# Kernel optimization log

Measured on AMD Instinct MI355X. Metric: run time of the kernel, lower is better.

Reference implementation:

```python
import jax, jax.numpy as jnp
import numpy as np

L, N, K, F, H = 6, 32768, 8, 32, 256  # levels, nodes/level, fan-in, feat_dim, hidden_dim


def setup_inputs() -> dict:
    key = jax.random.key(0)
    ks = jax.random.split(key, 10)
    sc = lambda k, shape, fan: (jax.random.normal(k, shape, jnp.float32) / np.sqrt(fan).astype(np.float32))
    return {
        "feats": jax.random.normal(ks[0], (L, N, F), jnp.float32),
        "pred_idx": jax.random.randint(ks[1], (L - 1, N, K), 0, N),
        "We": sc(ks[2], (H, F), F),
        "be": jnp.zeros((H,), jnp.float32),
        "rs_W1": sc(ks[3], (12, H, H), H),
        "rs_b1": jnp.zeros((12, H), jnp.float32),
        "rs_W2": sc(ks[4], (12, H, H), H),
        "rs_b2": jnp.zeros((12, H), jnp.float32),
        "rs_W3": sc(ks[5], (12, H, H), H),
        "rs_b3": jnp.zeros((12, H), jnp.float32),
        "rc_W1": sc(ks[6], (6, 2 * H, 2 * H), 2 * H),
        "rc_b1": jnp.zeros((6, 2 * H), jnp.float32),
        "rc_W2": sc(ks[7], (6, 2 * H, 2 * H), 2 * H),
        "rc_b2": jnp.zeros((6, 2 * H), jnp.float32),
        "rc_W3": sc(ks[8], (6, H, 2 * H), 2 * H),
        "rc_b3": jnp.zeros((6, H), jnp.float32),
    }


def _resnet(W1, b1, W2, b2, W3, b3, x):
    # lay3(tanh(lay2(tanh(lay1(x)))) + x)
    h1 = jnp.tanh(x @ W1.T + b1)
    h2 = jnp.tanh(h1 @ W2.T + b2)
    return (h2 + x) @ W3.T + b3


def reference(feats, pred_idx, We, be,
              rs_W1, rs_b1, rs_W2, rs_b2, rs_W3, rs_b3,
              rc_W1, rc_b1, rc_W2, rc_b2, rc_W3, rc_b3):
    # rs (h,h,h) order: [d1_mp, d1_mp1, d2_mp, d2_mp1, d3_mp, d3_mp1,
    #                    d1_node1, d2_node1, d3_node1, d1_comb1, d2_comb1, d3_comb1]
    # rc (2h,2h,h) order: [d1_node, d2_node, d3_node, d1_comb, d2_comb, d3_comb]
    small = lambda i, x: _resnet(rs_W1[i], rs_b1[i], rs_W2[i], rs_b2[i], rs_W3[i], rs_b3[i], x)
    big = lambda i, x: _resnet(rc_W1[i], rc_b1[i], rc_W2[i], rc_b2[i], rc_W3[i], rc_b3[i], x)

    n_levels = feats.shape[0]
    embeds = []
    for l in range(n_levels):  # sequential topological dependency (fixed, small L)
        e = jnp.tanh(feats[l] @ We.T + be)  # embed_op
        if l > 0:
            d = min(l - 1, 2)  # bwd_depth -> d1/d2/d3 branch
            # comb_embed branch: 'bwd_node_embeds' field exists but is DGL's
            # zero-initialized default for this frontier -> concat with zeros.
            x = jnp.concatenate([e, jnp.zeros_like(e)], axis=-1)
            e = jnp.tanh(small(9 + d, jnp.tanh(big(3 + d, x))))
            # message: gather predecessor embeds, sum-reduce, mp resnets
            msgs = jnp.sum(embeds[l - 1][pred_idx[l - 1]], axis=1)  # [N, H]
            r = jnp.tanh(small(2 * d, msgs))
            r = jnp.tanh(small(2 * d + 1, r))
            # node_embeds branch: concat(embeds, msgs_redux)
            x2 = jnp.concatenate([e, r], axis=-1)
            e = jnp.tanh(small(6 + d, jnp.tanh(big(d, x2))))
        embeds.append(e)
    return jnp.stack(embeds)  # graph.ndata['bwd_node_embeds'], [L, N, H]
```

## Files before the change

kernel.cpp:

```cpp
#include <hip/hip_runtime.h>

#define NLVL 6
#define NN   32768
#define KFAN 8
#define FDIM 32
#define HDIM 256

typedef __attribute__((ext_vector_type(4))) float f32x4;
typedef __attribute__((ext_vector_type(8))) _Float16 f16x8;
typedef __attribute__((ext_vector_type(4))) unsigned short u16x4;

__device__ __forceinline__ float h2f(unsigned short u) {
    _Float16 h; __builtin_memcpy(&h, &u, 2); return (float)h;
}
__device__ __forceinline__ unsigned short f2h(float f) {
    _Float16 h = (_Float16)f;
    unsigned short u; __builtin_memcpy(&u, &h, 2); return u;
}
__device__ __forceinline__ float tanh_fast(float x) {
    float e = __expf(2.0f * x);
    return 1.0f - 2.0f / (e + 1.0f);
}
__device__ __forceinline__ void gload16(const void* g, void* l) {
    __builtin_amdgcn_global_load_lds((const __attribute__((address_space(1))) void*)g,
                                     (__attribute__((address_space(3))) void*)l, 16, 0, 0);
}

template<bool RES, bool F32OUT>
__global__ __launch_bounds__(256)
void gemm_bt(const unsigned short* __restrict__ A, int lda,
             const unsigned short* __restrict__ B, int ldb,
             const float* __restrict__ bias,
             const unsigned short* __restrict__ res, int ldr,
             unsigned short* __restrict__ outB, int ldo,
             float* __restrict__ outF,
             int K)
{
    __shared__ __align__(16) unsigned short sA[128 * 64];
    __shared__ __align__(16) unsigned short sB[128 * 64];

    const int tid  = threadIdx.x;
    const int wid  = tid >> 6;
    const int lane = tid & 63;
    const int wr   = wid >> 1, wc = wid & 1;
    const int brow = blockIdx.x * 128;
    const int bcol = blockIdx.y * 128;
    const int fr   = lane & 15, fq = lane >> 4;
    const int srow = lane >> 3;
    const int scol = ((lane & 7) ^ srow) * 8;

    f32x4 acc[4][4] = {};

    for (int k0 = 0; k0 < K; k0 += 64) {
        #pragma unroll
        for (int it = 0; it < 4; ++it) {
            const int c = wid * 4 + it;
            const int r = c * 8 + srow;
            gload16(A + (size_t)(brow + r) * lda + k0 + scol, sA + c * 512);
            gload16(B + (size_t)(bcol + r) * ldb + k0 + scol, sB + c * 512);
        }
        __syncthreads();
        #pragma unroll
        for (int ks = 0; ks < 2; ++ks) {
            f16x8 av[4], bv[4];
            #pragma unroll
            for (int m = 0; m < 4; ++m) {
                const int r = wr * 64 + m * 16 + fr;
                const int b = r * 128 + ((ks * 64 + fq * 16) ^ ((r & 7) << 4));
                av[m] = *(const f16x8*)((const char*)sA + b);
            }
            #pragma unroll
            for (int n = 0; n < 4; ++n) {
                const int r = wc * 64 + n * 16 + fr;
                const int b = r * 128 + ((ks * 64 + fq * 16) ^ ((r & 7) << 4));
                bv[n] = *(const f16x8*)((const char*)sB + b);
            }
            #pragma unroll
            for (int m = 0; m < 4; ++m)
                #pragma unroll
                for (int n = 0; n < 4; ++n)
                    acc[m][n] = __builtin_amdgcn_mfma_f32_16x16x32_f16(av[m], bv[n], acc[m][n], 0, 0, 0);
        }
        __syncthreads();
    }

    #pragma unroll
    for (int m = 0; m < 4; ++m) {
        #pragma unroll
        for (int n = 0; n < 4; ++n) {
            const int col = bcol + wc * 64 + n * 16 + fr;
            const float bb = bias[col];
            #pragma unroll
            for (int j = 0; j < 4; ++j) {
                const int row = brow + wr * 64 + m * 16 + fq * 4 + j;
                float v = acc[m][n][j] + bb;
                v = tanh_fast(v);
                if (RES) v += h2f(res[(size_t)row * ldr + col]);
                outB[(size_t)row * ldo + col] = f2h(v);
                if (F32OUT) outF[(size_t)row * HDIM + col] = v;
            }
        }
    }
}

template<bool ZERO2, bool F32OUT>
__global__ __launch_bounds__(256)
void embed_kernel(const float* __restrict__ feats,
                  const float* __restrict__ We,
                  const float* __restrict__ be,
                  unsigned short* __restrict__ outB, int ldo,
                  float* __restrict__ outF)
{
    __shared__ float sW[256 * 33];
    __shared__ float sF[16 * 32];
    const int t = threadIdx.x;
    #pragma unroll
    for (int i = 0; i < 32; ++i) {
        int idx = t + 256 * i;
        sW[(idx >> 5) * 33 + (idx & 31)] = We[idx];
    }
    const size_t base = (size_t)blockIdx.x * 16;
    for (int i = t; i < 16 * 32; i += 256) sF[i] = feats[base * 32 + i];
    __syncthreads();

    const float bb = be[t];
    for (int r = 0; r < 16; ++r) {
        float a = bb;
        #pragma unroll
        for (int k = 0; k < 32; ++k) a += sF[r * 32 + k] * sW[t * 33 + k];
        const float v = tanh_fast(a);
        const size_t row = base + r;
        outB[row * ldo + t] = f2h(v);
        if (ZERO2) outB[row * ldo + 256 + t] = 0;
        if (F32OUT) outF[row * HDIM + t] = v;
    }
}

__global__ __launch_bounds__(256)
void gather_kernel(const unsigned short* __restrict__ ehalf,
                   const int* __restrict__ idx,
                   unsigned short* __restrict__ msg)
{
    const int n = blockIdx.x;
    const int t = threadIdx.x;
    const int* row = idx + (size_t)n * KFAN;
    float s = 0.f;
    #pragma unroll
    for (int k = 0; k < KFAN; ++k)
        s += h2f(ehalf[(size_t)row[k] * HDIM + t]);
    msg[(size_t)n * HDIM + t] = f2h(s);
}

__global__ __launch_bounds__(256)
void cvt_kernel(const float* __restrict__ in, unsigned short* __restrict__ out, int n4)
{
    const int i = blockIdx.x * 256 + threadIdx.x;
    if (i >= n4) return;
    const float4 v = ((const float4*)in)[i];
    u16x4 o;
    o[0] = f2h(v.x); o[1] = f2h(v.y); o[2] = f2h(v.z); o[3] = f2h(v.w);
    ((u16x4*)out)[i] = o;
}

extern "C" void kernel_launch(void* const* d_in, const int* in_sizes, int n_in,
                              void* d_out, int out_size, void* d_ws, size_t ws_size,
                              hipStream_t stream)
{
    const float* feats    = (const float*)d_in[0];
    const int*   pred_idx = (const int*)d_in[1];
    const float* We       = (const float*)d_in[2];
    const float* be       = (const float*)d_in[3];
    const float* rs_W1    = (const float*)d_in[4];
    const float* rs_b1    = (const float*)d_in[5];
    const float* rs_W2    = (const float*)d_in[6];
    const float* rs_b2    = (const float*)d_in[7];
    const float* rs_W3    = (const float*)d_in[8];
    const float* rs_b3    = (const float*)d_in[9];
    const float* rc_W1    = (const float*)d_in[10];
    const float* rc_b1    = (const float*)d_in[11];
    const float* rc_W2    = (const float*)d_in[12];
    const float* rc_b2    = (const float*)d_in[13];
    const float* rc_W3    = (const float*)d_in[14];
    const float* rc_b3    = (const float*)d_in[15];
    float* out = (float*)d_out;

    char* ws = (char*)d_ws;
    size_t off = 0;
    auto alloc = [&](size_t bytes) -> unsigned short* {
        unsigned short* p = (unsigned short*)(ws + off);
        off += (bytes + 255) & ~(size_t)255;
        return p;
    };
    unsigned short* rcW1b = alloc((size_t)6 * 512 * 512 * 2);
    unsigned short* rcW2b = alloc((size_t)6 * 512 * 512 * 2);
    unsigned short* rcW3b = alloc((size_t)6 * 256 * 512 * 2);
    unsigned short* rsW1b = alloc((size_t)12 * 256 * 256 * 2);
    unsigned short* rsW2b = alloc((size_t)12 * 256 * 256 * 2);
    unsigned short* rsW3b = alloc((size_t)12 * 256 * 256 * 2);
    unsigned short* xcat  = alloc((size_t)NN * 512 * 2);
    unsigned short* p0    = alloc((size_t)NN * 512 * 2);
    unsigned short* p1    = alloc((size_t)NN * 512 * 2);
    unsigned short* Tb    = alloc((size_t)NN * 256 * 2);
    unsigned short* q0    = alloc((size_t)NN * 256 * 2);
    unsigned short* q1    = alloc((size_t)NN * 256 * 2);
    unsigned short* msgb  = alloc((size_t)NN * 256 * 2);
    unsigned short* ebfA  = alloc((size_t)NN * 256 * 2);
    unsigned short* ebfB  = alloc((size_t)NN * 256 * 2);
    (void)ws_size; (void)in_sizes; (void)n_in; (void)out_size;

    auto cvt = [&](const float* src, unsigned short* dst, int n) {
        int n4 = n / 4;
        cvt_kernel<<<dim3((n4 + 255) / 256), dim3(256), 0, stream>>>(src, dst, n4);
    };
    cvt(rc_W1, rcW1b, 6 * 512 * 512);
    cvt(rc_W2, rcW2b, 6 * 512 * 512);
    cvt(rc_W3, rcW3b, 6 * 256 * 512);
    cvt(rs_W1, rsW1b, 12 * 256 * 256);
    cvt(rs_W2, rsW2b, 12 * 256 * 256);
    cvt(rs_W3, rsW3b, 12 * 256 * 256);

    auto G = [&](const unsigned short* Ap, int Kd, const unsigned short* Bp, int Nout,
                 const float* bp, const unsigned short* rp, int ldr,
                 unsigned short* ob, int ldo, float* of) {
        dim3 grid(NN / 128, Nout / 128);
        if (of)
            gemm_bt<false, true><<<grid, dim3(256), 0, stream>>>(Ap, Kd, Bp, Kd, bp, nullptr, 0, ob, ldo, of, Kd);
        else if (rp)
            gemm_bt<true, false><<<grid, dim3(256), 0, stream>>>(Ap, Kd, Bp, Kd, bp, rp, ldr, ob, ldo, nullptr, Kd);
        else
            gemm_bt<false, false><<<grid, dim3(256), 0, stream>>>(Ap, Kd, Bp, Kd, bp, nullptr, 0, ob, ldo, nullptr, Kd);
    };

    unsigned short* ebp = ebfA;
    unsigned short* ebc = ebfB;

    embed_kernel<false, true><<<dim3(NN / 16), dim3(256), 0, stream>>>(
        feats, We, be, ebp, 256, out);

    for (int l = 1; l < NLVL; ++l) {
        const int d = (l - 1 < 2) ? (l - 1) : 2;
        const float* fl = feats + (size_t)l * NN * FDIM;

        embed_kernel<true, false><<<dim3(NN / 16), dim3(256), 0, stream>>>(
            fl, We, be, xcat, 512, nullptr);

        G(xcat, 512, rcW1b + (size_t)(3 + d) * 512 * 512, 512, rc_b1 + (3 + d) * 512, nullptr, 0, p0, 512, nullptr);
        G(p0,   512, rcW2b + (size_t)(3 + d) * 512 * 512, 512, rc_b2 + (3 + d) * 512, xcat, 512,  p1, 512, nullptr);
        G(p1,   512, rcW3b + (size_t)(3 + d) * 256 * 512, 256, rc_b3 + (3 + d) * 256, nullptr, 0, Tb, 256, nullptr);
        G(Tb,   256, rsW1b + (size_t)(9 + d) * 256 * 256, 256, rs_b1 + (9 + d) * 256, nullptr, 0, q0, 256, nullptr);
        G(q0,   256, rsW2b + (size_t)(9 + d) * 256 * 256, 256, rs_b2 + (9 + d) * 256, Tb, 256,   q1, 256, nullptr);
        G(q1,   256, rsW3b + (size_t)(9 + d) * 256 * 256, 256, rs_b3 + (9 + d) * 256, nullptr, 0, p0, 512, nullptr);

        gather_kernel<<<dim3(NN), dim3(256), 0, stream>>>(
            ebp, pred_idx + (size_t)(l - 1) * NN * KFAN, msgb);
        G(msgb, 256, rsW1b + (size_t)(2 * d) * 256 * 256,     256, rs_b1 + (2 * d) * 256,     nullptr, 0, q0, 256, nullptr);
        G(q0,   256, rsW2b + (size_t)(2 * d) * 256 * 256,     256, rs_b2 + (2 * d) * 256,     msgb, 256,  q1, 256, nullptr);
        G(q1,   256, rsW3b + (size_t)(2 * d) * 256 * 256,     256, rs_b3 + (2 * d) * 256,     nullptr, 0, Tb, 256, nullptr);
        G(Tb,   256, rsW1b + (size_t)(2 * d + 1) * 256 * 256, 256, rs_b1 + (2 * d + 1) * 256, nullptr, 0, q0, 256, nullptr);
        G(q0,   256, rsW2b + (size_t)(2 * d + 1) * 256 * 256, 256, rs_b2 + (2 * d + 1) * 256, Tb, 256,   q1, 256, nullptr);
        G(q1,   256, rsW3b + (size_t)(2 * d + 1) * 256 * 256, 256, rs_b3 + (2 * d + 1) * 256, nullptr, 0, p0 + 256, 512, nullptr);

        G(p0,   512, rcW1b + (size_t)d * 512 * 512, 512, rc_b1 + d * 512, nullptr, 0, p1,   512, nullptr);
        G(p1,   512, rcW2b + (size_t)d * 512 * 512, 512, rc_b2 + d * 512, p0, 512,   xcat, 512, nullptr);
        G(xcat, 512, rcW3b + (size_t)d * 256 * 512, 256, rc_b3 + d * 256, nullptr, 0, Tb,  256, nullptr);
        G(Tb,   256, rsW1b + (size_t)(6 + d) * 256 * 256, 256, rs_b1 + (6 + d) * 256, nullptr, 0, q0, 256, nullptr);
        G(q0,   256, rsW2b + (size_t)(6 + d) * 256 * 256, 256, rs_b2 + (6 + d) * 256, Tb, 256,   q1, 256, nullptr);
        G(q1,   256, rsW3b + (size_t)(6 + d) * 256 * 256, 256, rs_b3 + (6 + d) * 256, nullptr, 0, ebc, 256,
          out + (size_t)l * NN * HDIM);

        unsigned short* tmp = ebp; ebp = ebc; ebc = tmp;
    }
}
```

Baseline: 2.073 ms.

## Fuse each three-layer resnet into one LDS-resident kernel with gather and zero-half skip

Replaces the per-layer GEMM launches with a single kernel per resnet block. The input tile and the hidden activations stay in shared memory across all three layers, and the weight fragments are read directly from global memory with double-buffered register prefetch. The predecessor gather-sum now runs inside the first message-passing resnet, and the big comb resnet uses K=256 because the concatenated second half is structurally zero. This removes most intermediate HBM round-trips and kernel launches, at the cost of large LDS footprints that limit occupancy and uncached global weight loads in the inner loop.

```diff
diff --git a/kernel.cpp b/kernel.cpp
--- a/kernel.cpp
+++ b/kernel.cpp
@@ -26,84 +26,183 @@
                                      (__attribute__((address_space(3))) void*)l, 16, 0, 0);
 }
 
-template<bool RES, bool F32OUT>
-__global__ __launch_bounds__(256)
-void gemm_bt(const unsigned short* __restrict__ A, int lda,
-             const unsigned short* __restrict__ B, int ldb,
-             const float* __restrict__ bias,
-             const unsigned short* __restrict__ res, int ldr,
-             unsigned short* __restrict__ outB, int ldo,
-             float* __restrict__ outF,
-             int K)
-{
-    __shared__ __align__(16) unsigned short sA[128 * 64];
-    __shared__ __align__(16) unsigned short sB[128 * 64];
-
-    const int tid  = threadIdx.x;
-    const int wid  = tid >> 6;
-    const int lane = tid & 63;
-    const int wr   = wid >> 1, wc = wid & 1;
-    const int brow = blockIdx.x * 128;
-    const int bcol = blockIdx.y * 128;
-    const int fr   = lane & 15, fq = lane >> 4;
-    const int srow = lane >> 3;
-    const int scol = ((lane & 7) ^ srow) * 8;
-
-    f32x4 acc[4][4] = {};
-
-    for (int k0 = 0; k0 < K; k0 += 64) {
-        #pragma unroll
-        for (int it = 0; it < 4; ++it) {
-            const int c = wid * 4 + it;
-            const int r = c * 8 + srow;
-            gload16(A + (size_t)(brow + r) * lda + k0 + scol, sA + c * 512);
-            gload16(B + (size_t)(bcol + r) * ldb + k0 + scol, sB + c * 512);
+template<int KLEN, int ROWB, int MFR>
+__device__ __forceinline__ void layer_mm(const unsigned short* sA,
+                                         const unsigned short* __restrict__ Wg, int ldw,
+                                         int rbase, int wcol, int lane,
+                                         f32x4 (&acc)[MFR][4])
+{
+    const int fr = lane & 15, fq = lane >> 4;
+    #pragma unroll
+    for (int m = 0; m < MFR; ++m)
+        #pragma unroll
+        for (int n = 0; n < 4; ++n)
+            acc[m][n] = (f32x4){0.f, 0.f, 0.f, 0.f};
+
+    constexpr int NKS = KLEN / 32;
+    f16x8 avA[MFR], avB[MFR], bvA[4], bvB[4];
+
+    auto ldB = [&](int ks, f16x8* bv) {
+        #pragma unroll
+        for (int n = 0; n < 4; ++n)
+            bv[n] = *(const f16x8*)(Wg + (size_t)(wcol + n * 16 + fr) * ldw + ks * 32 + fq * 8);
+    };
+    auto ldA = [&](int ks, f16x8* av) {
+        #pragma unroll
+        for (int m = 0; m < MFR; ++m) {
+            const int rr = rbase + m * 16 + fr;
+            const int byt = rr * ROWB + ((ks * 64 + fq * 16) ^ ((rr & 7) << 4));
+            av[m] = *(const f16x8*)((const char*)sA + byt);
         }
+    };
+    auto mm = [&](f16x8* av, f16x8* bv) {
+        #pragma unroll
+        for (int m = 0; m < MFR; ++m)
+            #pragma unroll
+            for (int n = 0; n < 4; ++n)
+                acc[m][n] = __builtin_amdgcn_mfma_f32_16x16x32_f16(av[m], bv[n], acc[m][n], 0, 0, 0);
+    };
+
+    ldA(0, avA); ldB(0, bvA);
+    #pragma unroll
+    for (int s = 0; s < NKS / 2; ++s) {
+        ldA(2 * s + 1, avB); ldB(2 * s + 1, bvB);
+        mm(avA, bvA);
+        if (2 * s + 2 < NKS) { ldA(2 * s + 2, avA); ldB(2 * s + 2, bvA); }
+        mm(avB, bvB);
+    }
+}
+
+template<int BM, int KD, int K1, bool GATHER, bool F32OUT>
+__global__ __launch_bounds__(512, 2)
+void resnet_fused(const unsigned short* __restrict__ X, int ldx,
+                  const int* __restrict__ gidx,
+                  const unsigned short* __restrict__ gsrc,
+                  const unsigned short* __restrict__ W1, const float* __restrict__ b1,
+                  const unsigned short* __restrict__ W2, const float* __restrict__ b2,
+                  const unsigned short* __restrict__ W3, const float* __restrict__ b3,
+                  unsigned short* __restrict__ outB, int ldo,
+                  float* __restrict__ outF)
+{
+    __shared__ __align__(16) unsigned short sX[BM * K1];
+    __shared__ __align__(16) unsigned short sH[BM * KD];
+    constexpr int ROWBX = K1 * 2, ROWBH = KD * 2;
+
+    const int tid = threadIdx.x, lane = tid & 63, wid = tid >> 6;
+    const int brow = blockIdx.x * BM;
+    const int fr = lane & 15, fq = lane >> 4;
+
+    if (GATHER) {
+        constexpr int CB = K1 / 8;
+        for (int i = tid; i < BM * CB; i += 512) {
+            const int row = i / CB, cb = i % CB;
+            const int* ip = gidx + (size_t)(brow + row) * KFAN;
+            float s[8] = {0.f, 0.f, 0.f, 0.f, 0.f, 0.f, 0.f, 0.f};
+            #pragma unroll
+            for (int k = 0; k < KFAN; ++k) {
+                f16x8 v = *(const f16x8*)(gsrc + (size_t)ip[k] * HDIM + cb * 8);
+                #pragma unroll
+                for (int j = 0; j < 8; ++j) s[j] += (float)v[j];
+            }
+            f16x8 o;
+            #pragma unroll
+            for (int j = 0; j < 8; ++j) o[j] = (_Float16)s[j];
+            *(f16x8*)((char*)sX + row * ROWBX + ((cb * 16) ^ ((row & 7) << 4))) = o;
+        }
+    } else {
+        constexpr int ROUNDS = BM * K1 * 2 / (512 * 16);
+        #pragma unroll
+        for (int r = 0; r < ROUNDS; ++r) {
+            const int lin = (r * 512 + tid) * 16;
+            const int row = lin / ROWBX;
+            const int cb  = (lin % ROWBX) >> 4;
+            const int scb = cb ^ (row & 7);
+            gload16(X + (size_t)(brow + row) * ldx + scb * 8,
+                    (char*)sX + (lin - lane * 16));
+        }
+    }
+    __syncthreads();
+
+    constexpr int NWC12 = KD / 64;
+    const int wc12 = (wid % NWC12) * 64;
+    const int rb12 = (wid / NWC12) * 64;
+    {
+        f32x4 a1[4][4];
+        layer_mm<K1, ROWBX, 4>(sX, W1, KD, rb12, wc12, lane, a1);
+        #pragma unroll
+        for (int m = 0; m < 4; ++m)
+            #pragma unroll
+            for (int n = 0; n < 4; ++n) {
+                const int col = wc12 + n * 16 + fr;
+                const float bb = b1[col];
+                #pragma unroll
+                for (int j = 0; j < 4; ++j) {
+                    const int row = rb12 + m * 16 + fq * 4 + j;
+                    const float v = tanh_fast(a1[m][n][j] + bb);
+                    *(unsigned short*)((char*)sH + row * ROWBH + ((col * 2) ^ ((row & 7) << 4))) = f2h(v);
+                }
+            }
+    }
+    __syncthreads();
+
+    {
+        f32x4 a2[4][4];
+        layer_mm<KD, ROWBH, 4>(sH, W2, KD, rb12, wc12, lane, a2);
+        #pragma unroll
+        for (int m = 0; m < 4; ++m)
+            #pragma unroll
+            for (int n = 0; n < 4; ++n) {
+                const int col = wc12 + n * 16 + fr;
+                const float bb = b2[col];
+                #pragma unroll
+                for (int j = 0; j < 4; ++j) {
+                    const int row = rb12 + m * 16 + fq * 4 + j;
+                    float v = tanh_fast(a2[m][n][j] + bb);
+                    if (col < K1)
+                        v += h2f(*(const unsigned short*)((const char*)sX + row * ROWBX + ((col * 2) ^ ((row & 7) << 4))));
+                    a2[m][n][j] = v;
+                }
+            }
         __syncthreads();
         #pragma unroll
-        for (int ks = 0; ks < 2; ++ks) {
-            f16x8 av[4], bv[4];
-            #pragma unroll
-            for (int m = 0; m < 4; ++m) {
-                const int r = wr * 64 + m * 16 + fr;
-                const int b = r * 128 + ((ks * 64 + fq * 16) ^ ((r & 7) << 4));
-                av[m] = *(const f16x8*)((const char*)sA + b);
-            }
+        for (int m = 0; m < 4; ++m)
             #pragma unroll
             for (int n = 0; n < 4; ++n) {
-                const int r = wc * 64 + n * 16 + fr;
-                const int b = r * 128 + ((ks * 64 + fq * 16) ^ ((r & 7) << 4));
-                bv[n] = *(const f16x8*)((const char*)sB + b);
-            }
-            #pragma unroll
-            for (int m = 0; m < 4; ++m)
-                #pragma unroll
-                for (int n = 0; n < 4; ++n)
-                    acc[m][n] = __builtin_amdgcn_mfma_f32_16x16x32_f16(av[m], bv[n], acc[m][n], 0, 0, 0);
-        }
-        __syncthreads();
-    }
-
-    #pragma unroll
-    for (int m = 0; m < 4; ++m) {
-        #pragma unroll
-        for (int n = 0; n < 4; ++n) {
-            const int col = bcol + wc * 64 + n * 16 + fr;
-            const float bb = bias[col];
-            #pragma unroll
-            for (int j = 0; j < 4; ++j) {
-                const int row = brow + wr * 64 + m * 16 + fq * 4 + j;
-                float v = acc[m][n][j] + bb;
-                v = tanh_fast(v);
-                if (RES) v += h2f(res[(size_t)row * ldr + col]);
-                outB[(size_t)row * ldo + col] = f2h(v);
-                if (F32OUT) outF[(size_t)row * HDIM + col] = v;
-            }
-        }
-    }
-}
-
-template<bool ZERO2, bool F32OUT>
+                const int col = wc12 + n * 16 + fr;
+                #pragma unroll
+                for (int j = 0; j < 4; ++j) {
+                    const int row = rb12 + m * 16 + fq * 4 + j;
+                    *(unsigned short*)((char*)sH + row * ROWBH + ((col * 2) ^ ((row & 7) << 4))) = f2h(a2[m][n][j]);
+                }
+            }
+    }
+    __syncthreads();
+
+    {
+        constexpr int WM3 = BM / 2, MFR3 = WM3 / 16;
+        const int wc3 = (wid & 3) * 64;
+        const int rb3 = (wid >> 2) * WM3;
+        f32x4 a3[MFR3][4];
+        layer_mm<KD, ROWBH, MFR3>(sH, W3, KD, rb3, wc3, lane, a3);
+        #pragma unroll
+        for (int m = 0; m < MFR3; ++m)
+            #pragma unroll
+            for (int n = 0; n < 4; ++n) {
+                const int col = wc3 + n * 16 + fr;
+                const float bb = b3[col];
+                #pragma unroll
+                for (int j = 0; j < 4; ++j) {
+                    const int row = rb3 + m * 16 + fq * 4 + j;
+                    const float v = tanh_fast(a3[m][n][j] + bb);
+                    const size_t gr = (size_t)(brow + row);
+                    outB[gr * ldo + col] = f2h(v);
+                    if (F32OUT) outF[gr * HDIM + col] = v;
+                }
+            }
+    }
+}
+
+template<bool F32OUT>
 __global__ __launch_bounds__(256)
 void embed_kernel(const float* __restrict__ feats,
                   const float* __restrict__ We,
@@ -131,24 +230,8 @@
         const float v = tanh_fast(a);
         const size_t row = base + r;
         outB[row * ldo + t] = f2h(v);
-        if (ZERO2) outB[row * ldo + 256 + t] = 0;
         if (F32OUT) outF[row * HDIM + t] = v;
     }
-}
-
-__global__ __launch_bounds__(256)
-void gather_kernel(const unsigned short* __restrict__ ehalf,
-                   const int* __restrict__ idx,
-                   unsigned short* __restrict__ msg)
-{
-    const int n = blockIdx.x;
-    const int t = threadIdx.x;
-    const int* row = idx + (size_t)n * KFAN;
-    float s = 0.f;
-    #pragma unroll
-    for (int k = 0; k < KFAN; ++k)
-        s += h2f(ehalf[(size_t)row[k] * HDIM + t]);
-    msg[(size_t)n * HDIM + t] = f2h(s);
 }
 
 __global__ __launch_bounds__(256)
@@ -197,13 +280,10 @@
     unsigned short* rsW1b = alloc((size_t)12 * 256 * 256 * 2);
     unsigned short* rsW2b = alloc((size_t)12 * 256 * 256 * 2);
     unsigned short* rsW3b = alloc((size_t)12 * 256 * 256 * 2);
-    unsigned short* xcat  = alloc((size_t)NN * 512 * 2);
+    unsigned short* xcat  = alloc((size_t)NN * 256 * 2);
     unsigned short* p0    = alloc((size_t)NN * 512 * 2);
-    unsigned short* p1    = alloc((size_t)NN * 512 * 2);
     unsigned short* Tb    = alloc((size_t)NN * 256 * 2);
     unsigned short* q0    = alloc((size_t)NN * 256 * 2);
-    unsigned short* q1    = alloc((size_t)NN * 256 * 2);
-    unsigned short* msgb  = alloc((size_t)NN * 256 * 2);
     unsigned short* ebfA  = alloc((size_t)NN * 256 * 2);
     unsigned short* ebfB  = alloc((size_t)NN * 256 * 2);
     (void)ws_size; (void)in_sizes; (void)n_in; (void)out_size;
@@ -219,54 +299,62 @@
     cvt(rs_W2, rsW2b, 12 * 256 * 256);
     cvt(rs_W3, rsW3b, 12 * 256 * 256);
 
-    auto G = [&](const unsigned short* Ap, int Kd, const unsigned short* Bp, int Nout,
-                 const float* bp, const unsigned short* rp, int ldr,
-                 unsigned short* ob, int ldo, float* of) {
-        dim3 grid(NN / 128, Nout / 128);
-        if (of)
-            gemm_bt<false, true><<<grid, dim3(256), 0, stream>>>(Ap, Kd, Bp, Kd, bp, nullptr, 0, ob, ldo, of, Kd);
-        else if (rp)
-            gemm_bt<true, false><<<grid, dim3(256), 0, stream>>>(Ap, Kd, Bp, Kd, bp, rp, ldr, ob, ldo, nullptr, Kd);
+    auto smallRN = [&](int i, const unsigned short* x, int ldx,
+                       unsigned short* ob, int ldo, float* of,
+                       const int* gidx, const unsigned short* gsrc) {
+        const unsigned short* w1 = rsW1b + (size_t)i * 256 * 256;
+        const unsigned short* w2 = rsW2b + (size_t)i * 256 * 256;
+        const unsigned short* w3 = rsW3b + (size_t)i * 256 * 256;
+        const float* B1 = rs_b1 + i * 256;
+        const float* B2 = rs_b2 + i * 256;
+        const float* B3 = rs_b3 + i * 256;
+        if (gidx)
+            resnet_fused<128, 256, 256, true, false><<<dim3(NN / 128), dim3(512), 0, stream>>>(
+                nullptr, 0, gidx, gsrc, w1, B1, w2, B2, w3, B3, ob, ldo, nullptr);
+        else if (of)
+            resnet_fused<128, 256, 256, false, true><<<dim3(NN / 128), dim3(512), 0, stream>>>(
+                x, ldx, nullptr, nullptr, w1, B1, w2, B2, w3, B3, ob, ldo, of);
         else
-            gemm_bt<false, false><<<grid, dim3(256), 0, stream>>>(Ap, Kd, Bp, Kd, bp, nullptr, 0, ob, ldo, nullptr, Kd);
+            resnet_fused<128, 256, 256, false, false><<<dim3(NN / 128), dim3(512), 0, stream>>>(
+                x, ldx, nullptr, nullptr, w1, B1, w2, B2, w3, B3, ob, ldo, nullptr);
+    };
+    auto bigRN = [&](int i, bool halfK, const unsigned short* x, int ldx, unsigned short* ob) {
+        const unsigned short* w1 = rcW1b + (size_t)i * 512 * 512;
+        const unsigned short* w2 = rcW2b + (size_t)i * 512 * 512;
+        const unsigned short* w3 = rcW3b + (size_t)i * 256 * 512;
+        const float* B1 = rc_b1 + i * 512;
+        const float* B2 = rc_b2 + i * 512;
+        const float* B3 = rc_b3 + i * 256;
+        if (halfK)
+            resnet_fused<64, 512, 256, false, false><<<dim3(NN / 64), dim3(512), 0, stream>>>(
+                x, ldx, nullptr, nullptr, w1, B1, w2, B2, w3, B3, ob, 256, nullptr);
+        else
+            resnet_fused<64, 512, 512, false, false><<<dim3(NN / 64), dim3(512), 0, stream>>>(
+                x, ldx, nullptr, nullptr, w1, B1, w2, B2, w3, B3, ob, 256, nullptr);
     };
 
     unsigned short* ebp = ebfA;
     unsigned short* ebc = ebfB;
 
-    embed_kernel<false, true><<<dim3(NN / 16), dim3(256), 0, stream>>>(
+    embed_kernel<true><<<dim3(NN / 16), dim3(256), 0, stream>>>(
         feats, We, be, ebp, 256, out);
 
     for (int l = 1; l < NLVL; ++l) {
         const int d = (l - 1 < 2) ? (l - 1) : 2;
         const float* fl = feats + (size_t)l * NN * FDIM;
-
-        embed_kernel<true, false><<<dim3(NN / 16), dim3(256), 0, stream>>>(
-            fl, We, be, xcat, 512, nullptr);
-
-        G(xcat, 512, rcW1b + (size_t)(3 + d) * 512 * 512, 512, rc_b1 + (3 + d) * 512, nullptr, 0, p0, 512, nullptr);
-        G(p0,   512, rcW2b + (size_t)(3 + d) * 512 * 512, 512, rc_b2 + (3 + d) * 512, xcat, 512,  p1, 512, nullptr);
-        G(p1,   512, rcW3b + (size_t)(3 + d) * 256 * 512, 256, rc_b3 + (3 + d) * 256, nullptr, 0, Tb, 256, nullptr);
-        G(Tb,   256, rsW1b + (size_t)(9 + d) * 256 * 256, 256, rs_b1 + (9 + d) * 256, nullptr, 0, q0, 256, nullptr);
-        G(q0,   256, rsW2b + (size_t)(9 + d) * 256 * 256, 256, rs_b2 + (9 + d) * 256, Tb, 256,   q1, 256, nullptr);
-        G(q1,   256, rsW3b + (size_t)(9 + d) * 256 * 256, 256, rs_b3 + (9 + d) * 256, nullptr, 0, p0, 512, nullptr);
-
-        gather_kernel<<<dim3(NN), dim3(256), 0, stream>>>(
-            ebp, pred_idx + (size_t)(l - 1) * NN * KFAN, msgb);
-        G(msgb, 256, rsW1b + (size_t)(2 * d) * 256 * 256,     256, rs_b1 + (2 * d) * 256,     nullptr, 0, q0, 256, nullptr);
-        G(q0,   256, rsW2b + (size_t)(2 * d) * 256 * 256,     256, rs_b2 + (2 * d) * 256,     msgb, 256,  q1, 256, nullptr);
-        G(q1,   256, rsW3b + (size_t)(2 * d) * 256 * 256,     256, rs_b3 + (2 * d) * 256,     nullptr, 0, Tb, 256, nullptr);
-        G(Tb,   256, rsW1b + (size_t)(2 * d + 1) * 256 * 256, 256, rs_b1 + (2 * d + 1) * 256, nullptr, 0, q0, 256, nullptr);
-        G(q0,   256, rsW2b + (size_t)(2 * d + 1) * 256 * 256, 256, rs_b2 + (2 * d + 1) * 256, Tb, 256,   q1, 256, nullptr);
-        G(q1,   256, rsW3b + (size_t)(2 * d + 1) * 256 * 256, 256, rs_b3 + (2 * d + 1) * 256, nullptr, 0, p0 + 256, 512, nullptr);
-
-        G(p0,   512, rcW1b + (size_t)d * 512 * 512, 512, rc_b1 + d * 512, nullptr, 0, p1,   512, nullptr);
-        G(p1,   512, rcW2b + (size_t)d * 512 * 512, 512, rc_b2 + d * 512, p0, 512,   xcat, 512, nullptr);
-        G(xcat, 512, rcW3b + (size_t)d * 256 * 512, 256, rc_b3 + d * 256, nullptr, 0, Tb,  256, nullptr);
-        G(Tb,   256, rsW1b + (size_t)(6 + d) * 256 * 256, 256, rs_b1 + (6 + d) * 256, nullptr, 0, q0, 256, nullptr);
-        G(q0,   256, rsW2b + (size_t)(6 + d) * 256 * 256, 256, rs_b2 + (6 + d) * 256, Tb, 256,   q1, 256, nullptr);
-        G(q1,   256, rsW3b + (size_t)(6 + d) * 256 * 256, 256, rs_b3 + (6 + d) * 256, nullptr, 0, ebc, 256,
-          out + (size_t)l * NN * HDIM);
+        const int* idx_l = pred_idx + (size_t)(l - 1) * NN * KFAN;
+
+        embed_kernel<false><<<dim3(NN / 16), dim3(256), 0, stream>>>(
+            fl, We, be, xcat, 256, nullptr);
+
+        bigRN(3 + d, true, xcat, 256, Tb);
+        smallRN(9 + d, Tb, 256, p0, 512, nullptr, nullptr, nullptr);
+
+        smallRN(2 * d,     nullptr, 0, q0, 256, nullptr, idx_l, ebp);
+        smallRN(2 * d + 1, q0, 256, p0 + 256, 512, nullptr, nullptr, nullptr);
+
+        bigRN(d, false, p0, 512, Tb);
+        smallRN(6 + d, Tb, 256, ebc, 256, out + (size_t)l * NN * HDIM, nullptr, nullptr);
 
         unsigned short* tmp = ebp; ebp = ebc; ebc = tmp;
     }
```

Result: slower. 2.159 ms (+4.2%).

## Batch independent comb and message GEMMs per launch and skip zero concat half

Applied to the files above, without the earlier changes.

Adds a descriptor-driven GEMM kernel that runs two independent GEMMs in one grid. The comb-embed branch and the message branch of each level now share launches instead of running back to back, which doubles the block count for the narrow 256-wide GEMMs and cuts launch count. The first comb GEMM now uses K=256 with the full-width weight stride, skipping the all-zero half of the concatenated input. Residual adds are limited to the first 256 columns, and all level embeddings are computed in one launch up front. The cost is a runtime branch on descriptor fields inside the GEMM epilogue and some extra workspace buffers.

```diff
diff --git a/kernel.cpp b/kernel.cpp
--- a/kernel.cpp
+++ b/kernel.cpp
@@ -26,16 +26,25 @@
                                      (__attribute__((address_space(3))) void*)l, 16, 0, 0);
 }
 
-template<bool RES, bool F32OUT>
-__global__ __launch_bounds__(256)
-void gemm_bt(const unsigned short* __restrict__ A, int lda,
-             const unsigned short* __restrict__ B, int ldb,
-             const float* __restrict__ bias,
-             const unsigned short* __restrict__ res, int ldr,
-             unsigned short* __restrict__ outB, int ldo,
-             float* __restrict__ outF,
-             int K)
-{
+struct GDesc {
+    const unsigned short* A;
+    const unsigned short* B;
+    const float* bias;
+    const unsigned short* res;
+    unsigned short* outB;
+    float* outF;
+    int lda, ldb, ldr, ldo, resW, K, nblk;
+};
+
+__global__ __launch_bounds__(256)
+void gemm_batch(GDesc d0, GDesc d1, int nblk0)
+{
+    const bool sec = (int)blockIdx.x >= nblk0;
+    const GDesc& d = sec ? d1 : d0;
+    const int bx = sec ? ((int)blockIdx.x - nblk0) : (int)blockIdx.x;
+    const int brow = (bx & 255) * 128;
+    const int bcol = (bx >> 8) * 128;
+
     __shared__ __align__(16) unsigned short sA[128 * 64];
     __shared__ __align__(16) unsigned short sB[128 * 64];
 
@@ -43,12 +52,11 @@
     const int wid  = tid >> 6;
     const int lane = tid & 63;
     const int wr   = wid >> 1, wc = wid & 1;
-    const int brow = blockIdx.x * 128;
-    const int bcol = blockIdx.y * 128;
     const int fr   = lane & 15, fq = lane >> 4;
     const int srow = lane >> 3;
     const int scol = ((lane & 7) ^ srow) * 8;
 
+    const int lda = d.lda, ldb = d.ldb, K = d.K;
     f32x4 acc[4][4] = {};
 
     for (int k0 = 0; k0 < K; k0 += 64) {
@@ -56,8 +64,8 @@
         for (int it = 0; it < 4; ++it) {
             const int c = wid * 4 + it;
             const int r = c * 8 + srow;
-            gload16(A + (size_t)(brow + r) * lda + k0 + scol, sA + c * 512);
-            gload16(B + (size_t)(bcol + r) * ldb + k0 + scol, sB + c * 512);
+            gload16(d.A + (size_t)(brow + r) * lda + k0 + scol, sA + c * 512);
+            gload16(d.B + (size_t)(bcol + r) * ldb + k0 + scol, sB + c * 512);
         }
         __syncthreads();
         #pragma unroll
@@ -84,45 +92,49 @@
         __syncthreads();
     }
 
+    const unsigned short* res = d.res;
     #pragma unroll
     for (int m = 0; m < 4; ++m) {
         #pragma unroll
         for (int n = 0; n < 4; ++n) {
             const int col = bcol + wc * 64 + n * 16 + fr;
-            const float bb = bias[col];
+            const float bb = d.bias[col];
             #pragma unroll
             for (int j = 0; j < 4; ++j) {
                 const int row = brow + wr * 64 + m * 16 + fq * 4 + j;
                 float v = acc[m][n][j] + bb;
                 v = tanh_fast(v);
-                if (RES) v += h2f(res[(size_t)row * ldr + col]);
-                outB[(size_t)row * ldo + col] = f2h(v);
-                if (F32OUT) outF[(size_t)row * HDIM + col] = v;
+                if (res && col < d.resW) v += h2f(res[(size_t)row * d.ldr + col]);
+                d.outB[(size_t)row * d.ldo + col] = f2h(v);
+                if (d.outF) d.outF[(size_t)row * HDIM + col] = v;
             }
         }
     }
 }
 
-template<bool ZERO2, bool F32OUT>
-__global__ __launch_bounds__(256)
-void embed_kernel(const float* __restrict__ feats,
-                  const float* __restrict__ We,
-                  const float* __restrict__ be,
-                  unsigned short* __restrict__ outB, int ldo,
-                  float* __restrict__ outF)
+__global__ __launch_bounds__(256)
+void embed_all(const float* __restrict__ feats,
+               const float* __restrict__ We,
+               const float* __restrict__ be,
+               unsigned short* __restrict__ ebuf,
+               float* __restrict__ out0)
 {
     __shared__ float sW[256 * 33];
     __shared__ float sF[16 * 32];
+    const int l   = blockIdx.x >> 11;
+    const int blk = blockIdx.x & 2047;
     const int t = threadIdx.x;
     #pragma unroll
     for (int i = 0; i < 32; ++i) {
         int idx = t + 256 * i;
         sW[(idx >> 5) * 33 + (idx & 31)] = We[idx];
     }
-    const size_t base = (size_t)blockIdx.x * 16;
-    for (int i = t; i < 16 * 32; i += 256) sF[i] = feats[base * 32 + i];
+    const size_t base = (size_t)blk * 16;
+    const float* fl = feats + (size_t)l * NN * FDIM;
+    for (int i = t; i < 16 * 32; i += 256) sF[i] = fl[base * 32 + i];
     __syncthreads();
 
+    unsigned short* ob = ebuf + (size_t)l * NN * HDIM;
     const float bb = be[t];
     for (int r = 0; r < 16; ++r) {
         float a = bb;
@@ -130,9 +142,8 @@
         for (int k = 0; k < 32; ++k) a += sF[r * 32 + k] * sW[t * 33 + k];
         const float v = tanh_fast(a);
         const size_t row = base + r;
-        outB[row * ldo + t] = f2h(v);
-        if (ZERO2) outB[row * ldo + 256 + t] = 0;
-        if (F32OUT) outF[row * HDIM + t] = v;
+        ob[row * HDIM + t] = f2h(v);
+        if (l == 0) out0[row * HDIM + t] = v;
     }
 }
 
@@ -170,17 +181,11 @@
     const int*   pred_idx = (const int*)d_in[1];
     const float* We       = (const float*)d_in[2];
     const float* be       = (const float*)d_in[3];
-    const float* rs_W1    = (const float*)d_in[4];
     const float* rs_b1    = (const float*)d_in[5];
-    const float* rs_W2    = (const float*)d_in[6];
     const float* rs_b2    = (const float*)d_in[7];
-    const float* rs_W3    = (const float*)d_in[8];
     const float* rs_b3    = (const float*)d_in[9];
-    const float* rc_W1    = (const float*)d_in[10];
     const float* rc_b1    = (const float*)d_in[11];
-    const float* rc_W2    = (const float*)d_in[12];
     const float* rc_b2    = (const float*)d_in[13];
-    const float* rc_W3    = (const float*)d_in[14];
     const float* rc_b3    = (const float*)d_in[15];
     float* out = (float*)d_out;
 
@@ -197,12 +202,15 @@
     unsigned short* rsW1b = alloc((size_t)12 * 256 * 256 * 2);
     unsigned short* rsW2b = alloc((size_t)12 * 256 * 256 * 2);
     unsigned short* rsW3b = alloc((size_t)12 * 256 * 256 * 2);
-    unsigned short* xcat  = alloc((size_t)NN * 512 * 2);
+    unsigned short* ebuf  = alloc((size_t)NLVL * NN * 256 * 2);
     unsigned short* p0    = alloc((size_t)NN * 512 * 2);
     unsigned short* p1    = alloc((size_t)NN * 512 * 2);
+    unsigned short* p2    = alloc((size_t)NN * 512 * 2);
     unsigned short* Tb    = alloc((size_t)NN * 256 * 2);
     unsigned short* q0    = alloc((size_t)NN * 256 * 2);
     unsigned short* q1    = alloc((size_t)NN * 256 * 2);
+    unsigned short* q2    = alloc((size_t)NN * 256 * 2);
+    unsigned short* q3    = alloc((size_t)NN * 256 * 2);
     unsigned short* msgb  = alloc((size_t)NN * 256 * 2);
     unsigned short* ebfA  = alloc((size_t)NN * 256 * 2);
     unsigned short* ebfB  = alloc((size_t)NN * 256 * 2);
@@ -212,62 +220,70 @@
         int n4 = n / 4;
         cvt_kernel<<<dim3((n4 + 255) / 256), dim3(256), 0, stream>>>(src, dst, n4);
     };
-    cvt(rc_W1, rcW1b, 6 * 512 * 512);
-    cvt(rc_W2, rcW2b, 6 * 512 * 512);
-    cvt(rc_W3, rcW3b, 6 * 256 * 512);
-    cvt(rs_W1, rsW1b, 12 * 256 * 256);
-    cvt(rs_W2, rsW2b, 12 * 256 * 256);
-    cvt(rs_W3, rsW3b, 12 * 256 * 256);
-
-    auto G = [&](const unsigned short* Ap, int Kd, const unsigned short* Bp, int Nout,
-                 const float* bp, const unsigned short* rp, int ldr,
-                 unsigned short* ob, int ldo, float* of) {
-        dim3 grid(NN / 128, Nout / 128);
-        if (of)
-            gemm_bt<false, true><<<grid, dim3(256), 0, stream>>>(Ap, Kd, Bp, Kd, bp, nullptr, 0, ob, ldo, of, Kd);
-        else if (rp)
-            gemm_bt<true, false><<<grid, dim3(256), 0, stream>>>(Ap, Kd, Bp, Kd, bp, rp, ldr, ob, ldo, nullptr, Kd);
-        else
-            gemm_bt<false, false><<<grid, dim3(256), 0, stream>>>(Ap, Kd, Bp, Kd, bp, nullptr, 0, ob, ldo, nullptr, Kd);
-    };
-
-    unsigned short* ebp = ebfA;
-    unsigned short* ebc = ebfB;
-
-    embed_kernel<false, true><<<dim3(NN / 16), dim3(256), 0, stream>>>(
-        feats, We, be, ebp, 256, out);
+    cvt((const float*)d_in[10], rcW1b, 6 * 512 * 512);
+    cvt((const float*)d_in[12], rcW2b, 6 * 512 * 512);
+    cvt((const float*)d_in[14], rcW3b, 6 * 256 * 512);
+    cvt((const float*)d_in[4],  rsW1b, 12 * 256 * 256);
+    cvt((const float*)d_in[6],  rsW2b, 12 * 256 * 256);
+    cvt((const float*)d_in[8],  rsW3b, 12 * 256 * 256);
+
+    embed_all<<<dim3(NLVL * (NN / 16)), dim3(256), 0, stream>>>(feats, We, be, ebuf, out);
+
+    auto D = [&](const unsigned short* A, int lda, const unsigned short* B, int ldb,
+                 int N, int K, const float* bias,
+                 const unsigned short* res, int ldr, int resW,
+                 unsigned short* ob, int ldo, float* of) -> GDesc {
+        GDesc g;
+        g.A = A; g.B = B; g.bias = bias; g.res = res; g.outB = ob; g.outF = of;
+        g.lda = lda; g.ldb = ldb; g.ldr = ldr; g.ldo = ldo; g.resW = resW;
+        g.K = K; g.nblk = 256 * (N / 128);
+        return g;
+    };
+    GDesc Z; Z.nblk = 0;
+    auto GB = [&](const GDesc& a, const GDesc& b) {
+        gemm_batch<<<dim3(a.nblk + b.nblk), dim3(256), 0, stream>>>(a, b, a.nblk);
+    };
+
+    const unsigned short* ep = ebuf;
+    unsigned short* ebc = ebfA;
+    unsigned short* ebn = ebfB;
 
     for (int l = 1; l < NLVL; ++l) {
         const int d = (l - 1 < 2) ? (l - 1) : 2;
-        const float* fl = feats + (size_t)l * NN * FDIM;
-
-        embed_kernel<true, false><<<dim3(NN / 16), dim3(256), 0, stream>>>(
-            fl, We, be, xcat, 512, nullptr);
-
-        G(xcat, 512, rcW1b + (size_t)(3 + d) * 512 * 512, 512, rc_b1 + (3 + d) * 512, nullptr, 0, p0, 512, nullptr);
-        G(p0,   512, rcW2b + (size_t)(3 + d) * 512 * 512, 512, rc_b2 + (3 + d) * 512, xcat, 512,  p1, 512, nullptr);
-        G(p1,   512, rcW3b + (size_t)(3 + d) * 256 * 512, 256, rc_b3 + (3 + d) * 256, nullptr, 0, Tb, 256, nullptr);
-        G(Tb,   256, rsW1b + (size_t)(9 + d) * 256 * 256, 256, rs_b1 + (9 + d) * 256, nullptr, 0, q0, 256, nullptr);
-        G(q0,   256, rsW2b + (size_t)(9 + d) * 256 * 256, 256, rs_b2 + (9 + d) * 256, Tb, 256,   q1, 256, nullptr);
-        G(q1,   256, rsW3b + (size_t)(9 + d) * 256 * 256, 256, rs_b3 + (9 + d) * 256, nullptr, 0, p0, 512, nullptr);
-
-        gather_kernel<<<dim3(NN), dim3(256), 0, stream>>>(
-            ebp, pred_idx + (size_t)(l - 1) * NN * KFAN, msgb);
-        G(msgb, 256, rsW1b + (size_t)(2 * d) * 256 * 256,     256, rs_b1 + (2 * d) * 256,     nullptr, 0, q0, 256, nullptr);
-        G(q0,   256, rsW2b + (size_t)(2 * d) * 256 * 256,     256, rs_b2 + (2 * d) * 256,     msgb, 256,  q1, 256, nullptr);
-        G(q1,   256, rsW3b + (size_t)(2 * d) * 256 * 256,     256, rs_b3 + (2 * d) * 256,     nullptr, 0, Tb, 256, nullptr);
-        G(Tb,   256, rsW1b + (size_t)(2 * d + 1) * 256 * 256, 256, rs_b1 + (2 * d + 1) * 256, nullptr, 0, q0, 256, nullptr);
-        G(q0,   256, rsW2b + (size_t)(2 * d + 1) * 256 * 256, 256, rs_b2 + (2 * d + 1) * 256, Tb, 256,   q1, 256, nullptr);
-        G(q1,   256, rsW3b + (size_t)(2 * d + 1) * 256 * 256, 256, rs_b3 + (2 * d + 1) * 256, nullptr, 0, p0 + 256, 512, nullptr);
-
-        G(p0,   512, rcW1b + (size_t)d * 512 * 512, 512, rc_b1 + d * 512, nullptr, 0, p1,   512, nullptr);
-        G(p1,   512, rcW2b + (size_t)d * 512 * 512, 512, rc_b2 + d * 512, p0, 512,   xcat, 512, nullptr);
-        G(xcat, 512, rcW3b + (size_t)d * 256 * 512, 256, rc_b3 + d * 256, nullptr, 0, Tb,  256, nullptr);
-        G(Tb,   256, rsW1b + (size_t)(6 + d) * 256 * 256, 256, rs_b1 + (6 + d) * 256, nullptr, 0, q0, 256, nullptr);
-        G(q0,   256, rsW2b + (size_t)(6 + d) * 256 * 256, 256, rs_b2 + (6 + d) * 256, Tb, 256,   q1, 256, nullptr);
-        G(q1,   256, rsW3b + (size_t)(6 + d) * 256 * 256, 256, rs_b3 + (6 + d) * 256, nullptr, 0, ebc, 256,
-          out + (size_t)l * NN * HDIM);
-
-        unsigned short* tmp = ebp; ebp = ebc; ebc = tmp;
-    }
-}
+        const unsigned short* el = ebuf + (size_t)l * NN * 256;
+        const int* idx_l = pred_idx + (size_t)(l - 1) * NN * KFAN;
+
+        const unsigned short* cw1 = rcW1b + (size_t)(3 + d) * 512 * 512;
+        const unsigned short* cw2 = rcW2b + (size_t)(3 + d) * 512 * 512;
+        const unsigned short* cw3 = rcW3b + (size_t)(3 + d) * 256 * 512;
+        const unsigned short* nw1 = rcW1b + (size_t)d * 512 * 512;
+        const unsigned short* nw2 = rcW2b + (size_t)d * 512 * 512;
+        const unsigned short* nw3 = rcW3b + (size_t)d * 256 * 512;
+        auto sw = [&](const unsigned short* base, int i) { return base + (size_t)i * 256 * 256; };
+
+        gather_kernel<<<dim3(NN), dim3(256), 0, stream>>>(ep, idx_l, msgb);
+
+        GB(D(el, 256, cw1, 512, 512, 256, rc_b1 + (3 + d) * 512, nullptr, 0, 0, p1, 512, nullptr),
+           D(msgb, 256, sw(rsW1b, 2 * d), 256, 256, 256, rs_b1 + (2 * d) * 256, nullptr, 0, 0, q0, 256, nullptr));
+        GB(D(p1, 512, cw2, 512, 512, 512, rc_b2 + (3 + d) * 512, el, 256, 256, p2, 512, nullptr),
+           D(q0, 256, sw(rsW2b, 2 * d), 256, 256, 256, rs_b2 + (2 * d) * 256, msgb, 256, 256, q1, 256, nullptr));
+        GB(D(p2, 512, cw3, 512, 256, 512, rc_b3 + (3 + d) * 256, nullptr, 0, 0, Tb, 256, nullptr),
+           D(q1, 256, sw(rsW3b, 2 * d), 256, 256, 256, rs_b3 + (2 * d) * 256, nullptr, 0, 0, q2, 256, nullptr));
+        GB(D(Tb, 256, sw(rsW1b, 9 + d), 256, 256, 256, rs_b1 + (9 + d) * 256, nullptr, 0, 0, q0, 256, nullptr),
+           D(q2, 256, sw(rsW1b, 2 * d + 1), 256, 256, 256, rs_b1 + (2 * d + 1) * 256, nullptr, 0, 0, q3, 256, nullptr));
+        GB(D(q0, 256, sw(rsW2b, 9 + d), 256, 256, 256, rs_b2 + (9 + d) * 256, Tb, 256, 256, q1, 256, nullptr),
+           D(q3, 256, sw(rsW2b, 2 * d + 1), 256, 256, 256, rs_b2 + (2 * d + 1) * 256, q2, 256, 256, msgb, 256, nullptr));
+        GB(D(q1, 256, sw(rsW3b, 9 + d), 256, 256, 256, rs_b3 + (9 + d) * 256, nullptr, 0, 0, p0, 512, nullptr),
+           D(msgb, 256, sw(rsW3b, 2 * d + 1), 256, 256, 256, rs_b3 + (2 * d + 1) * 256, nullptr, 0, 0, p0 + 256, 512, nullptr));
+        GB(D(p0, 512, nw1, 512, 512, 512, rc_b1 + d * 512, nullptr, 0, 0, p1, 512, nullptr), Z);
+        GB(D(p1, 512, nw2, 512, 512, 512, rc_b2 + d * 512, p0, 512, 512, p2, 512, nullptr), Z);
+        GB(D(p2, 512, nw3, 512, 256, 512, rc_b3 + d * 256, nullptr, 0, 0, Tb, 256, nullptr), Z);
+        GB(D(Tb, 256, sw(rsW1b, 6 + d), 256, 256, 256, rs_b1 + (6 + d) * 256, nullptr, 0, 0, q0, 256, nullptr), Z);
+        GB(D(q0, 256, sw(rsW2b, 6 + d), 256, 256, 256, rs_b2 + (6 + d) * 256, Tb, 256, 256, q1, 256, nullptr), Z);
+        GB(D(q1, 256, sw(rsW3b, 6 + d), 256, 256, 256, rs_b3 + (6 + d) * 256, nullptr, 0, 0, ebc, 256,
+             out + (size_t)l * NN * HDIM), Z);
+
+        ep = ebc;
+        unsigned short* t = ebc; ebc = ebn; ebn = t;
+    }
+}
```

Result: slower. 2.608 ms (+25.8%).
